# Kernel optimization log

Measured on AMD Instinct MI355X. Metric: run time of the kernel, lower is better.

## Reference

```python
import jax, jax.numpy as jnp
import numpy as np

B, S, I, H, O = 256, 512, 128, 256, 1


def setup_inputs() -> dict:
    key = jax.random.key(0)
    ks = jax.random.split(key, 12)
    s_a = 1.0 / np.sqrt(H + I)
    s_g = 1.0 / np.sqrt(H)
    s_f = 1.0 / np.sqrt(H)
    return {
        "x": jax.random.normal(ks[0], (B, S, I), dtype=jnp.float32),
        # input attention linear: (H+I) -> I
        "W_a": jax.random.uniform(ks[1], (I, H + I), minval=-s_a, maxval=s_a),
        "b_a": jax.random.uniform(ks[2], (I,), minval=-s_a, maxval=s_a),
        # GRUCell params (torch layout: [3H, I] / [3H, H], gate order r,z,n)
        "W_ih": jax.random.uniform(ks[3], (3 * H, I), minval=-s_g, maxval=s_g),
        "b_ih": jax.random.uniform(ks[4], (3 * H,), minval=-s_g, maxval=s_g),
        "W_hh": jax.random.uniform(ks[5], (3 * H, H), minval=-s_g, maxval=s_g),
        "b_hh": jax.random.uniform(ks[6], (3 * H,), minval=-s_g, maxval=s_g),
        # temporal attention linear: H -> 1
        "W_t": jax.random.uniform(ks[7], (1, H), minval=-s_f, maxval=s_f),
        "b_t": jax.random.uniform(ks[8], (1,), minval=-s_f, maxval=s_f),
        # output fc: H -> O
        "W_f": jax.random.uniform(ks[9], (O, H), minval=-s_f, maxval=s_f),
        "b_f": jax.random.uniform(ks[10], (O,), minval=-s_f, maxval=s_f),
    }


def reference(x, W_a, b_a, W_ih, b_ih, W_hh, b_hh, W_t, b_t, W_f, b_f):
    def step(h, x_t):  # h: [B,H], x_t: [B,I]
        combined = jnp.concatenate([x_t, h], axis=1)            # [B, I+H]
        scores = jnp.tanh(combined @ W_a.T + b_a)               # [B, I]
        alpha = jax.nn.softmax(scores, axis=1)                  # [B, I]
        xw = alpha * x_t                                        # [B, I]
        gi = xw @ W_ih.T + b_ih                                 # [B, 3H]
        gh = h @ W_hh.T + b_hh                                  # [B, 3H]
        i_r, i_z, i_n = jnp.split(gi, 3, axis=1)
        h_r, h_z, h_n = jnp.split(gh, 3, axis=1)
        r = jax.nn.sigmoid(i_r + h_r)
        z = jax.nn.sigmoid(i_z + h_z)
        n = jnp.tanh(i_n + r * h_n)
        h_new = (1.0 - z) * n + z * h
        return h_new, h_new

    h0 = jnp.zeros((x.shape[0], W_hh.shape[1]), dtype=x.dtype)
    xs = jnp.transpose(x, (1, 0, 2))                            # [S,B,I]
    _, hs = jax.lax.scan(step, h0, xs)                          # hs: [S,B,H]
    enc = jnp.transpose(hs, (1, 0, 2))                          # [B,S,H]

    t_scores = jnp.tanh(enc @ W_t.T + b_t)                      # [B,S,1]
    beta = jax.nn.softmax(t_scores, axis=1)                     # softmax over time
    context = jnp.sum(beta * enc, axis=1)                       # [B,H]
    logits = context @ W_f.T + b_f                              # [B,O]
    return jax.nn.sigmoid(logits)
```

## Files before the change

### kernel.cpp

```cpp
#include <hip/hip_runtime.h>
#include <math.h>

#define BB 256
#define SS 512
#define II 128
#define HH 256

typedef unsigned short ushort_t;
typedef unsigned int uint32;

#define OFF_WA   0
#define OFF_BA   49152
#define OFF_WIH  49280
#define OFF_BIH  147584
#define OFF_WHH  148352
#define OFF_BHH  344960
#define OFF_WT   345728
#define OFF_BT   345984
#define OFF_WF   345992
#define OFF_BF   346248
#define OFF_WAH  346256
#define OFF_GIX  379024

#define WHH_LC   12

__device__ __forceinline__ float h2f(ushort_t u) {
    union { ushort_t s[2]; _Float16 h[2]; } v; v.s[0] = u; return (float)v.h[0];
}
__device__ __forceinline__ ushort_t f2h(float f) {
    union { _Float16 h; ushort_t s; } v; v.h = (_Float16)f; return v.s;
}
__device__ __forceinline__ uint32 pack2(float a, float b) {
    union { _Float16 h[2]; uint32 u; } v;
    v.h[0] = (_Float16)a; v.h[1] = (_Float16)b; return v.u;
}

#if __has_builtin(__builtin_amdgcn_fdot2)
typedef _Float16 v2h __attribute__((ext_vector_type(2)));
__device__ __forceinline__ float dot2u(uint32 w, uint32 v, float acc) {
    return __builtin_amdgcn_fdot2(
        __builtin_bit_cast(v2h, w), __builtin_bit_cast(v2h, v), acc, false);
}
#else
__device__ __forceinline__ float dot2u(uint32 w, uint32 v, float acc) {
    union { uint32 u; _Float16 h[2]; } a, b; a.u = w; b.u = v;
    acc = fmaf((float)a.h[0], (float)b.h[0], acc);
    return fmaf((float)a.h[1], (float)b.h[1], acc);
}
#endif
__device__ __forceinline__ float dot4(uint4 w, uint4 v, float acc) {
    acc = dot2u(w.x, v.x, acc); acc = dot2u(w.y, v.y, acc);
    acc = dot2u(w.z, v.z, acc); return dot2u(w.w, v.w, acc);
}

__global__ void cvt_f32_f16(const float* __restrict__ src, ushort_t* __restrict__ dst, int n) {
    int i = blockIdx.x * 256 + threadIdx.x;
    if (i < n) dst[i] = f2h(src[i]);
}

__global__ void cvt_swz(const float* __restrict__ src, ushort_t* __restrict__ dst,
                        int rows, int chunks, int srcStride, int colOff) {
    int t = blockIdx.x * 256 + threadIdx.x;
    if (t >= rows * chunks) return;
    int row = t / chunks, c = t % chunks;
    const float* s = src + (size_t)row * srcStride + colOff + c * 8;
    uint4 v;
    v.x = pack2(s[0], s[1]); v.y = pack2(s[2], s[3]);
    v.z = pack2(s[4], s[5]); v.w = pack2(s[6], s[7]);
    ((uint4*)dst)[((size_t)(row >> 6) * chunks + c) * 64 + (row & 63)] = v;
}

__global__ __launch_bounds__(512, 2) void gix_kernel(
    const float* __restrict__ x, const ushort_t* __restrict__ wsb,
    float* __restrict__ gix)
{
    const int b = blockIdx.x, tid = threadIdx.x;
    const int r4 = tid >> 7, i = tid & 127;
    __shared__ __align__(16) uint32 sxp[4][64];

    uint4 w[16];
    const uint4* wa_g = (const uint4*)(wsb + OFF_WA);
    const size_t gb = (size_t)(i >> 6) * 48 * 64 + (i & 63);
    #pragma unroll
    for (int c = 0; c < 16; ++c) w[c] = wa_g[gb + (size_t)c * 64];

    const float* xb = x + (size_t)b * SS * II;
    float* gout = gix + (size_t)b * SS * II;
    for (int j = 0; j < SS; j += 4) {
        float v = xb[(j + r4) * II + i];
        float vn = __shfl_down(v, 1);
        if (!(i & 1)) sxp[r4][i >> 1] = pack2(v, vn);
        __syncthreads();
        const uint4* sx4 = (const uint4*)sxp[r4];
        float acc = 0.f;
        #pragma unroll
        for (int c = 0; c < 16; ++c) acc = dot4(w[c], sx4[c], acc);
        gout[(j + r4) * II + i] = acc;
        __syncthreads();
    }
}

template <int GIX>
__global__ __launch_bounds__(1024, 4) void da_rnn_kernel(
    const float* __restrict__ x,
    const ushort_t* __restrict__ wsb,
    const float* __restrict__ gix,
    float* __restrict__ out)
{
    const int b    = blockIdx.x;
    const int tid  = threadIdx.x;
    const int lane = tid & 63;
    const int wv   = tid >> 6;
    const bool is_gate = (tid < 3 * HH);

    __shared__ __align__(16) uint32 whh_lds[WHH_LC * 768 * 4];
    __shared__ __align__(16) uint32 s_xh_p[192];
    __shared__ __align__(16) uint32 sxw_p[64];
    __shared__ __align__(16) float  sred[256];
    __shared__ __align__(16) float  sgi[3 * HH];
    __shared__ __align__(16) float  sgh[3 * HH];
    __shared__ __align__(16) float  sx[2][II];
    __shared__ __align__(16) float  sgix[2][II];
    __shared__ float swave[4];
    __shared__ int   flag_red;
    __shared__ int   flag_xw;

    if (tid == 0) { flag_red = 0; flag_xw = 0; }
    if (tid < II) s_xh_p[64 + tid] = 0u;

    uint4 wreg[16];
    const int a   = tid - 3 * HH;
    const int row = a & 127;
    const int s   = a >> 7;
    const uint4* whh_base = (const uint4*)(wsb + OFF_WHH) + (size_t)wv * 32 * 64 + lane;
    const uint4* wa_st = nullptr;
    float bias_i = 0.f, bias_h = 0.f, ba_a = 0.f, ba_b = 0.f;

    if (is_gate) {
        const uint4* wih_g = (const uint4*)(wsb + OFF_WIH) + (size_t)wv * 16 * 64 + lane;
        #pragma unroll
        for (int c = 0; c < 16; ++c) wreg[c] = wih_g[c * 64];
        bias_i = h2f(wsb[OFF_BIH + tid]);
        bias_h = h2f(wsb[OFF_BHH + tid]);
        #pragma unroll
        for (int c = 0; c < WHH_LC; ++c)
            ((uint4*)whh_lds)[(wv * WHH_LC + c) * 64 + lane] = whh_base[c * 64];
    } else {
        if (GIX) {
            const uint4* wah_g = (const uint4*)(wsb + OFF_WAH);
            const size_t gbh = ((size_t)(row >> 6) * 32 + s * 16) * 64 + (row & 63);
            #pragma unroll
            for (int i = 0; i < 16; ++i) wreg[i] = wah_g[gbh + (size_t)i * 64];
        } else {
            const uint4* wa_g = (const uint4*)(wsb + OFF_WA);
            const size_t gbase = ((size_t)(row >> 6) * 48 + s * 24) * 64 + (row & 63);
            #pragma unroll
            for (int i = 0; i < 16; ++i) wreg[i] = wa_g[gbase + (size_t)i * 64];
            wa_st = wa_g + gbase + (size_t)16 * 64;
        }
        ba_a = h2f(wsb[OFF_BA + lane]);
        ba_b = h2f(wsb[OFF_BA + 64 + lane]);
    }

    float h_reg = 0.f, c_reg = 0.f, m_run = -2.0f, l_run = 0.f;
    float wt_j = 0.f, wf_j = 0.f, bt_r = 0.f;
    if (tid < HH) {
        wt_j = h2f(wsb[OFF_WT + tid]);
        wf_j = h2f(wsb[OFF_WF + tid]);
        bt_r = h2f(wsb[OFF_BT]);
    }

    const float* xrow  = x + (size_t)b * SS * II;
    const float* grow0 = GIX ? (gix + (size_t)b * SS * II) : nullptr;
    if (!is_gate && a >= 64 && a < 192) {
        const int idx = a - 64;
        float v = xrow[idx];
        sx[0][idx] = v;
        if (!GIX) {
            float vn = __shfl_down(v, 1);
            if (!(idx & 1)) s_xh_p[idx >> 1] = pack2(v, vn);
        }
    }
    if (GIX && !is_gate && a >= 192) {
        const int l = a - 192;
        sgix[0][l]      = grow0[l];
        sgix[0][64 + l] = grow0[64 + l];
    }
    __syncthreads();

    const uint4* st4 = (const uint4*)s_xh_p;
    const uint4* shp = (const uint4*)s_xh_p + 16;
    const uint4* xwp = (const uint4*)sxw_p;
    const uint4* whl = (const uint4*)whh_lds + (size_t)(wv * WHH_LC) * 64 + lane;

    for (int t = 0; t < SS; ++t) {
        const int p = t & 1;

        if (is_gate) {
            float gh = bias_h;
            #pragma unroll
            for (int c = 0; c < WHH_LC; ++c) gh = dot4(whl[c * 64], shp[c], gh);
            #pragma unroll 4
            for (int c = WHH_LC; c < 32; ++c) gh = dot4(whh_base[c * 64], shp[c], gh);
            sgh[tid] = gh;
            while (__hip_atomic_load(&flag_xw, __ATOMIC_ACQUIRE,
                                     __HIP_MEMORY_SCOPE_WORKGROUP) <= t) {}
            float gi = bias_i;
            #pragma unroll
            for (int c = 0; c < 16; ++c) gi = dot4(wreg[c], xwp[c], gi);
            sgi[tid] = gi;
        } else {
            float acc;
            if (GIX) {
                acc = 0.f;
                #pragma unroll
                for (int i = 0; i < 16; ++i) acc = dot4(wreg[i], shp[s * 16 + i], acc);
            } else {
                acc = 0.f;
                #pragma unroll
                for (int i = 0; i < 16; ++i) acc = dot4(wreg[i], st4[s * 24 + i], acc);
                #pragma unroll 4
                for (int i = 0; i < 8; ++i) acc = dot4(wa_st[i * 64], st4[s * 24 + 16 + i], acc);
            }
            sred[a] = acc;
            if (lane == 0)
                __hip_atomic_fetch_add(&flag_red, 1, __ATOMIC_ACQ_REL,
                                       __HIP_MEMORY_SCOPE_WORKGROUP);
            const int tgt = 4 * (t + 1);
            while (__hip_atomic_load(&flag_red, __ATOMIC_ACQUIRE,
                                     __HIP_MEMORY_SCOPE_WORKGROUP) < tgt) {}
            if (a < 64) {
                float s_a = sred[lane] + sred[128 + lane] + ba_a;
                float s_b = sred[64 + lane] + sred[192 + lane] + ba_b;
                if (GIX) { s_a += sgix[p][lane]; s_b += sgix[p][64 + lane]; }
                s_a = tanhf(s_a); s_b = tanhf(s_b);
                float m = fmaxf(s_a, s_b);
                for (int off = 32; off; off >>= 1) m = fmaxf(m, __shfl_xor(m, off));
                float e_a = expf(s_a - m), e_b = expf(s_b - m);
                float sum = e_a + e_b;
                for (int off = 32; off; off >>= 1) sum += __shfl_xor(sum, off);
                float inv = 1.f / sum;
                float xa = e_a * inv * sx[p][lane];
                float xb = e_b * inv * sx[p][64 + lane];
                float xa1 = __shfl_down(xa, 1), xb1 = __shfl_down(xb, 1);
                if (!(lane & 1)) {
                    sxw_p[lane >> 1]        = pack2(xa, xa1);
                    sxw_p[32 + (lane >> 1)] = pack2(xb, xb1);
                }
                if (lane == 0)
                    __hip_atomic_store(&flag_xw, t + 1, __ATOMIC_RELEASE,
                                       __HIP_MEMORY_SCOPE_WORKGROUP);
            } else if (a >= 64 && a < 192 && t + 1 < SS) {
                const int idx = a - 64;
                float v = xrow[(t + 1) * II + idx];
                sx[p ^ 1][idx] = v;
                if (!GIX) {
                    float vn = __shfl_down(v, 1);
                    if (!(idx & 1)) s_xh_p[idx >> 1] = pack2(v, vn);
                }
            } else if (GIX && a >= 192 && t + 1 < SS) {
                const float* gr = grow0 + (size_t)(t + 1) * II;
                const int l = a - 192;
                sgix[p ^ 1][l]      = gr[l];
                sgix[p ^ 1][64 + l] = gr[64 + l];
            }
        }
        __syncthreads();

        if (tid < HH) {
            const float r = 1.f / (1.f + expf(-(sgi[tid] + sgh[tid])));
            const float z = 1.f / (1.f + expf(-(sgi[tid + HH] + sgh[tid + HH])));
            const float n = tanhf(sgi[tid + 2 * HH] + r * sgh[tid + 2 * HH]);
            h_reg = (1.f - z) * n + z * h_reg;
            float hn2 = __shfl_down(h_reg, 1);
            if (!(tid & 1)) s_xh_p[64 + (tid >> 1)] = pack2(h_reg, hn2);
            float pd = wt_j * h_reg;
            for (int off = 32; off; off >>= 1) pd += __shfl_down(pd, off);
            if (lane == 0) swave[wv] = pd;
        }
        __syncthreads();

        if (tid < HH) {
            float dot = swave[0] + swave[1] + swave[2] + swave[3] + bt_r;
            float st = tanhf(dot);
            float mn = fmaxf(m_run, st);
            float aa = expf(m_run - mn), ww = expf(st - mn);
            l_run = l_run * aa + ww;
            m_run = mn;
            c_reg = c_reg * aa + ww * h_reg;
        }
    }

    __syncthreads();
    if (tid < HH) {
        float ctx = c_reg / l_run;
        float pd = wf_j * ctx;
        for (int off = 32; off; off >>= 1) pd += __shfl_down(pd, off);
        if (lane == 0) swave[wv] = pd;
    }
    __syncthreads();
    if (tid == 0) {
        float logit = swave[0] + swave[1] + swave[2] + swave[3] + h2f(wsb[OFF_BF]);
        out[b] = 1.f / (1.f + expf(-logit));
    }
}

extern "C" void kernel_launch(void* const* d_in, const int* in_sizes, int n_in,
                              void* d_out, int out_size, void* d_ws, size_t ws_size,
                              hipStream_t stream) {
    ushort_t* wsb = (ushort_t*)d_ws;
    const size_t WS_NEED = (size_t)OFF_GIX * 2 + (size_t)BB * SS * II * 4;
    const bool use_gix = ws_size >= WS_NEED;

    cvt_swz<<<dim3((128 * 48 + 255) / 256), dim3(256), 0, stream>>>(
        (const float*)d_in[1], wsb + OFF_WA, 128, 48, 384, 0);
    cvt_swz<<<dim3((768 * 16 + 255) / 256), dim3(256), 0, stream>>>(
        (const float*)d_in[3], wsb + OFF_WIH, 768, 16, 128, 0);
    cvt_swz<<<dim3((768 * 32 + 255) / 256), dim3(256), 0, stream>>>(
        (const float*)d_in[5], wsb + OFF_WHH, 768, 32, 256, 0);
    if (use_gix)
        cvt_swz<<<dim3((128 * 32 + 255) / 256), dim3(256), 0, stream>>>(
            (const float*)d_in[1], wsb + OFF_WAH, 128, 32, 384, 128);

    struct { int src_idx; int off; int n; } cv[7] = {
        {2, OFF_BA,  II}, {4, OFF_BIH, 3 * HH}, {6, OFF_BHH, 3 * HH},
        {7, OFF_WT,  HH}, {8, OFF_BT, 1}, {9, OFF_WF, HH}, {10, OFF_BF, 1},
    };
    for (int i = 0; i < 7; ++i) {
        int blocks = (cv[i].n + 255) / 256;
        cvt_f32_f16<<<dim3(blocks), dim3(256), 0, stream>>>(
            (const float*)d_in[cv[i].src_idx], wsb + cv[i].off, cv[i].n);
    }

    float* gixf = (float*)(wsb + OFF_GIX);
    if (use_gix) {
        gix_kernel<<<dim3(BB), dim3(512), 0, stream>>>(
            (const float*)d_in[0], wsb, gixf);
        da_rnn_kernel<1><<<dim3(BB), dim3(1024), 0, stream>>>(
            (const float*)d_in[0], wsb, gixf, (float*)d_out);
    } else {
        da_rnn_kernel<0><<<dim3(BB), dim3(1024), 0, stream>>>(
            (const float*)d_in[0], wsb, nullptr, (float*)d_out);
    }
}
```

Measured before the change: 2.394 ms.

## Offload part of W_hh recurrent matvec to idle attention waves

```diff
diff --git a/kernel.cpp b/kernel.cpp
--- a/kernel.cpp
+++ b/kernel.cpp
@@ -100,12 +100,237 @@
     }
 }
 
-template <int GIX>
-__global__ __launch_bounds__(1024, 4) void da_rnn_kernel(
+__global__ __launch_bounds__(1024, 4) void da_rnn_s_kernel(
     const float* __restrict__ x,
     const ushort_t* __restrict__ wsb,
     const float* __restrict__ gix,
     float* __restrict__ out)
+{
+    const int b    = blockIdx.x;
+    const int tid  = threadIdx.x;
+    const int lane = tid & 63;
+    const int wv   = tid >> 6;
+    const bool is_gate = (tid < 3 * HH);
+
+    __shared__ __align__(16) uint32 whh_lds[WHH_LC * 768 * 4];
+    __shared__ __align__(16) uint32 s_xh_p[192];
+    __shared__ __align__(16) uint32 sxw_p[64];
+    __shared__ __align__(16) float  sred[256];
+    __shared__ __align__(16) float  sgi[3 * HH];
+    __shared__ __align__(16) float  sgh[3 * HH];
+    __shared__ __align__(16) float  sgh2[3 * HH];
+    __shared__ __align__(16) float  sx[2][II];
+    __shared__ __align__(16) float  sgix[2][II];
+    __shared__ float swave[4];
+    __shared__ int   flag_red;
+    __shared__ int   flag_xw;
+
+    if (tid == 0) { flag_red = 0; flag_xw = 0; }
+    if (tid < II) s_xh_p[64 + tid] = 0u;
+
+    uint4 wreg[16];
+    const int a = tid - 3 * HH;
+    const uint4* whh_base = (const uint4*)(wsb + OFF_WHH) + (size_t)wv * 32 * 64 + lane;
+    float bias_i = 0.f, bias_h = 0.f, ba_a = 0.f, ba_b = 0.f;
+
+    if (is_gate) {
+        const uint4* wih_g = (const uint4*)(wsb + OFF_WIH) + (size_t)wv * 16 * 64 + lane;
+        #pragma unroll
+        for (int c = 0; c < 16; ++c) wreg[c] = wih_g[c * 64];
+        bias_i = h2f(wsb[OFF_BIH + tid]);
+        bias_h = h2f(wsb[OFF_BHH + tid]);
+        #pragma unroll
+        for (int c = 0; c < WHH_LC; ++c)
+            ((uint4*)whh_lds)[(wv * WHH_LC + c) * 64 + lane] = whh_base[c * 64];
+    } else {
+        const int row = a & 127;
+        const int s   = a >> 7;
+        const uint4* wah_g = (const uint4*)(wsb + OFF_WAH);
+        const size_t gbh = ((size_t)(row >> 6) * 32 + s * 16) * 64 + (row & 63);
+        #pragma unroll
+        for (int i = 0; i < 16; ++i) wreg[i] = wah_g[gbh + (size_t)i * 64];
+        ba_a = h2f(wsb[OFF_BA + lane]);
+        ba_b = h2f(wsb[OFF_BA + 64 + lane]);
+    }
+
+    float h_reg = 0.f, c_reg = 0.f, m_run = -2.0f, l_run = 0.f;
+    float wt_j = 0.f, wf_j = 0.f, bt_r = 0.f;
+    if (tid < HH) {
+        wt_j = h2f(wsb[OFF_WT + tid]);
+        wf_j = h2f(wsb[OFF_WF + tid]);
+        bt_r = h2f(wsb[OFF_BT]);
+    }
+
+    const float* xrow  = x   + (size_t)b * SS * II;
+    const float* grow0 = gix + (size_t)b * SS * II;
+    if (!is_gate && a >= 64 && a < 192) {
+        const int idx = a - 64;
+        sx[0][idx] = xrow[idx];
+    }
+    if (!is_gate && a >= 192) {
+        const int l = a - 192;
+        sgix[0][l]      = grow0[l];
+        sgix[0][64 + l] = grow0[64 + l];
+    }
+    __syncthreads();
+
+    const uint4* shp = (const uint4*)s_xh_p + 16;
+    const uint4* xwp = (const uint4*)sxw_p;
+    const uint4* whl = (const uint4*)whh_lds + (size_t)(wv * WHH_LC) * 64 + lane;
+
+    for (int t = 0; t < SS; ++t) {
+        const int p = t & 1;
+
+        if (is_gate) {
+            float g0 = bias_h, g1 = 0.f;
+            #pragma unroll
+            for (int c = 0; c < WHH_LC; c += 2) {
+                g0 = dot4(whl[(c + 0) * 64], shp[c + 0], g0);
+                g1 = dot4(whl[(c + 1) * 64], shp[c + 1], g1);
+            }
+            #pragma unroll 5
+            for (int c = WHH_LC; c < 22; c += 2) {
+                g0 = dot4(whh_base[(c + 0) * 64], shp[c + 0], g0);
+                g1 = dot4(whh_base[(c + 1) * 64], shp[c + 1], g1);
+            }
+            sgh[tid] = g0 + g1;
+            while (__hip_atomic_load(&flag_xw, __ATOMIC_ACQUIRE,
+                                     __HIP_MEMORY_SCOPE_WORKGROUP) <= t)
+                __builtin_amdgcn_s_sleep(1);
+            float q0 = bias_i, q1 = 0.f;
+            #pragma unroll
+            for (int c = 0; c < 16; c += 2) {
+                q0 = dot4(wreg[c + 0], xwp[c + 0], q0);
+                q1 = dot4(wreg[c + 1], xwp[c + 1], q1);
+            }
+            sgi[tid] = q0 + q1;
+        } else {
+            const int s = a >> 7;
+            float p0 = 0.f, p1 = 0.f;
+            #pragma unroll
+            for (int i = 0; i < 16; i += 2) {
+                p0 = dot4(wreg[i + 0], shp[s * 16 + i + 0], p0);
+                p1 = dot4(wreg[i + 1], shp[s * 16 + i + 1], p1);
+            }
+            sred[a] = p0 + p1;
+            if (lane == 0)
+                __hip_atomic_fetch_add(&flag_red, 1, __ATOMIC_ACQ_REL,
+                                       __HIP_MEMORY_SCOPE_WORKGROUP);
+
+            if ((a >= 64 && a < 128) || a >= 192) {
+                const int k = (a < 128) ? (a - 64) : (64 + (a - 192));
+                const uint4* wst = (const uint4*)(wsb + OFF_WHH)
+                                 + (size_t)(k >> 6) * 2048 + (k & 63);
+                float a0 = 0.f, a1 = 0.f, a2 = 0.f, a3 = 0.f, a4 = 0.f;
+                #pragma unroll 2
+                for (int c = 22; c < 32; ++c) {
+                    a0 = dot4(wst[c * 64],         shp[c], a0);
+                    a1 = dot4(wst[4096 + c * 64],  shp[c], a1);
+                    a2 = dot4(wst[8192 + c * 64],  shp[c], a2);
+                    a3 = dot4(wst[12288 + c * 64], shp[c], a3);
+                    a4 = dot4(wst[16384 + c * 64], shp[c], a4);
+                }
+                sgh2[k]       = a0;
+                sgh2[k + 128] = a1;
+                sgh2[k + 256] = a2;
+                sgh2[k + 384] = a3;
+                sgh2[k + 512] = a4;
+                if (t + 1 < SS) {
+                    const size_t o = (size_t)(t + 1) * II;
+                    if (a < 128) {
+                        const int l = a - 64;
+                        sx[p ^ 1][l]      = xrow[o + l];
+                        sx[p ^ 1][64 + l] = xrow[o + 64 + l];
+                    } else {
+                        const int l = a - 192;
+                        sgix[p ^ 1][l]      = grow0[o + l];
+                        sgix[p ^ 1][64 + l] = grow0[o + 64 + l];
+                    }
+                }
+            } else if (a >= 128) {
+                const int k2 = a - 128;
+                const uint4* wst = (const uint4*)(wsb + OFF_WHH)
+                                 + (size_t)10 * 2048 + k2;
+                float a0 = 0.f, a1 = 0.f;
+                #pragma unroll 2
+                for (int c = 22; c < 32; ++c) {
+                    a0 = dot4(wst[c * 64],        shp[c], a0);
+                    a1 = dot4(wst[2048 + c * 64], shp[c], a1);
+                }
+                sgh2[640 + k2] = a0;
+                sgh2[704 + k2] = a1;
+            } else {
+                while (__hip_atomic_load(&flag_red, __ATOMIC_ACQUIRE,
+                                         __HIP_MEMORY_SCOPE_WORKGROUP) < 4 * (t + 1))
+                    __builtin_amdgcn_s_sleep(1);
+                float s_a = sred[lane] + sred[128 + lane] + sgix[p][lane] + ba_a;
+                float s_b = sred[64 + lane] + sred[192 + lane] + sgix[p][64 + lane] + ba_b;
+                s_a = tanhf(s_a); s_b = tanhf(s_b);
+                float m = fmaxf(s_a, s_b);
+                for (int off = 32; off; off >>= 1) m = fmaxf(m, __shfl_xor(m, off));
+                float e_a = expf(s_a - m), e_b = expf(s_b - m);
+                float sum = e_a + e_b;
+                for (int off = 32; off; off >>= 1) sum += __shfl_xor(sum, off);
+                float inv = 1.f / sum;
+                float xa = e_a * inv * sx[p][lane];
+                float xb = e_b * inv * sx[p][64 + lane];
+                float xa1 = __shfl_down(xa, 1), xb1 = __shfl_down(xb, 1);
+                if (!(lane & 1)) {
+                    sxw_p[lane >> 1]        = pack2(xa, xa1);
+                    sxw_p[32 + (lane >> 1)] = pack2(xb, xb1);
+                }
+                if (lane == 0)
+                    __hip_atomic_store(&flag_xw, t + 1, __ATOMIC_RELEASE,
+                                       __HIP_MEMORY_SCOPE_WORKGROUP);
+            }
+        }
+        __syncthreads();
+
+        if (tid < HH) {
+            const float ghr = sgh[tid]          + sgh2[tid];
+            const float ghz = sgh[tid + HH]     + sgh2[tid + HH];
+            const float ghn = sgh[tid + 2 * HH] + sgh2[tid + 2 * HH];
+            const float r = 1.f / (1.f + expf(-(sgi[tid] + ghr)));
+            const float z = 1.f / (1.f + expf(-(sgi[tid + HH] + ghz)));
+            const float n = tanhf(sgi[tid + 2 * HH] + r * ghn);
+            h_reg = (1.f - z) * n + z * h_reg;
+            float hn2 = __shfl_down(h_reg, 1);
+            if (!(tid & 1)) s_xh_p[64 + (tid >> 1)] = pack2(h_reg, hn2);
+            float pd = wt_j * h_reg;
+            for (int off = 32; off; off >>= 1) pd += __shfl_down(pd, off);
+            if (lane == 0) swave[wv] = pd;
+        }
+        __syncthreads();
+
+        if (tid < HH) {
+            float dot = swave[0] + swave[1] + swave[2] + swave[3] + bt_r;
+            float st = tanhf(dot);
+            float mn = fmaxf(m_run, st);
+            float aa = expf(m_run - mn), ww = expf(st - mn);
+            l_run = l_run * aa + ww;
+            m_run = mn;
+            c_reg = c_reg * aa + ww * h_reg;
+        }
+    }
+
+    __syncthreads();
+    if (tid < HH) {
+        float ctx = c_reg / l_run;
+        float pd = wf_j * ctx;
+        for (int off = 32; off; off >>= 1) pd += __shfl_down(pd, off);
+        if (lane == 0) swave[wv] = pd;
+    }
+    __syncthreads();
+    if (tid == 0) {
+        float logit = swave[0] + swave[1] + swave[2] + swave[3] + h2f(wsb[OFF_BF]);
+        out[b] = 1.f / (1.f + expf(-logit));
+    }
+}
+
+template <int GIX>
+__global__ __launch_bounds__(1024, 4) void da_rnn_kernel(
+    const float* __restrict__ x, const ushort_t* __restrict__ wsb,
+    const float* __restrict__ gix, float* __restrict__ out)
 {
     const int b    = blockIdx.x;
     const int tid  = threadIdx.x;
@@ -204,7 +429,8 @@
             for (int c = WHH_LC; c < 32; ++c) gh = dot4(whh_base[c * 64], shp[c], gh);
             sgh[tid] = gh;
             while (__hip_atomic_load(&flag_xw, __ATOMIC_ACQUIRE,
-                                     __HIP_MEMORY_SCOPE_WORKGROUP) <= t) {}
+                                     __HIP_MEMORY_SCOPE_WORKGROUP) <= t)
+                __builtin_amdgcn_s_sleep(1);
             float gi = bias_i;
             #pragma unroll
             for (int c = 0; c < 16; ++c) gi = dot4(wreg[c], xwp[c], gi);
@@ -228,7 +454,8 @@
                                        __HIP_MEMORY_SCOPE_WORKGROUP);
             const int tgt = 4 * (t + 1);
             while (__hip_atomic_load(&flag_red, __ATOMIC_ACQUIRE,
-                                     __HIP_MEMORY_SCOPE_WORKGROUP) < tgt) {}
+                                     __HIP_MEMORY_SCOPE_WORKGROUP) < tgt)
+                __builtin_amdgcn_s_sleep(1);
             if (a < 64) {
                 float s_a = sred[lane] + sred[128 + lane] + ba_a;
                 float s_b = sred[64 + lane] + sred[192 + lane] + ba_b;
@@ -336,7 +563,7 @@
     if (use_gix) {
         gix_kernel<<<dim3(BB), dim3(512), 0, stream>>>(
             (const float*)d_in[0], wsb, gixf);
-        da_rnn_kernel<1><<<dim3(BB), dim3(1024), 0, stream>>>(
+        da_rnn_s_kernel<<<dim3(BB), dim3(1024), 0, stream>>>(
             (const float*)d_in[0], wsb, gixf, (float*)d_out);
     } else {
         da_rnn_kernel<0><<<dim3(BB), dim3(1024), 0, stream>>>(
```

New measurement: 4.249 ms. +77.5%, slower.
